# Kernel optimization log

Measured on AMD Instinct MI355X. Metric: run time of the kernel, lower is better.

## Reference

```python
import jax, jax.numpy as jnp
import numpy as np


def _diff_x(x, r):
    left = x[:, r:2 * r + 1]
    middle = x[:, 2 * r + 1:] - x[:, :-2 * r - 1]
    right = x[:, -1:] - x[:, -2 * r - 1:-r - 1]
    return jnp.concatenate([left, middle, right], axis=1)


def _diff_y(x, r):
    left = x[:, :, r:2 * r + 1]
    middle = x[:, :, 2 * r + 1:] - x[:, :, :-2 * r - 1]
    right = x[:, :, -1:] - x[:, :, -2 * r - 1:-r - 1]
    return jnp.concatenate([left, middle, right], axis=2)


def _box_filter(x, r):
    # Sliding box sum via cumsum+diff along H then W (NHWC)
    return _diff_y(jnp.cumsum(_diff_x(jnp.cumsum(x, axis=1), r), axis=2), r)


def setup_inputs() -> dict:
    key = jax.random.key(0)
    k1, k2 = jax.random.split(key)
    B, H, W, C = 4, 1024, 1024, 4
    I = jax.random.uniform(k1, (B, H, W, C), dtype=jnp.float32)
    p = jax.random.uniform(k2, (B, H, W, C), dtype=jnp.float32)
    return {"I": I, "p": p, "r": 40}


def reference(I, p, r):
    eps = 1e-08
    _, H, W, _ = I.shape
    N = _box_filter(jnp.ones((1, H, W, 1), dtype=I.dtype), r)  # box area per pixel
    mean_I = _box_filter(I, r) / N
    mean_p = _box_filter(p, r) / N
    cov_Ip = _box_filter(I * p, r) / N - mean_I * mean_p
    var_I = _box_filter(I * I, r) / N - mean_I * mean_I
    A = cov_Ip / (var_I + eps)
    b = mean_p - A * mean_I
    mean_A = _box_filter(A, r) / N
    mean_b = _box_filter(b, r) / N
    q = mean_A * I + mean_b
    return q
```

## Files before the change

kernel.cpp:

```cpp
#include <hip/hip_runtime.h>
#include <hip/hip_fp16.h>


#define HD 1024
#define WD 1024
#define ROW4 WD
#define IMG4 ((size_t)HD * ROW4)
#define IMGF (IMG4 * 4)
#define BH 16
#define NB (HD / BH)
#define CH 16
#define NCH (HD / CH)
#define TPB 256
#define PPT 4
#define PFXN 1153
#define EPS 1e-8f

__device__ __forceinline__ int idx4(int p) { return p + (p >> 3); }

__device__ __forceinline__ void barrier_lds() {
    asm volatile("s_waitcnt lgkmcnt(0)" ::: "memory");
    __builtin_amdgcn_s_barrier();
}

struct H4 { __half2 lo, hi; };

__device__ __forceinline__ H4 pack4(float4 v) {
    H4 h; h.lo = __floats2half2_rn(v.x, v.y); h.hi = __floats2half2_rn(v.z, v.w);
    return h;
}
__device__ __forceinline__ float4 unpack4(H4 h) {
    float2 l = __half22float2(h.lo), u = __half22float2(h.hi);
    return make_float4(l.x, l.y, u.x, u.y);
}
__device__ __forceinline__ float4 packAB(H4 a, H4 b) {
    union { H4 h[2]; float4 f; } u; u.h[0] = a; u.h[1] = b; return u.f;
}
__device__ __forceinline__ float4 f4add(float4 a, float4 b) {
    return make_float4(a.x + b.x, a.y + b.y, a.z + b.z, a.w + b.w);
}
__device__ __forceinline__ float4 f4sub(float4 a, float4 b) {
    return make_float4(a.x - b.x, a.y - b.y, a.z - b.z, a.w - b.w);
}
__device__ __forceinline__ float4 f4s(float4 a, float s) {
    return make_float4(a.x * s, a.y * s, a.z * s, a.w * s);
}
__device__ __forceinline__ float4 f4mul(float4 a, float4 b) {
    return make_float4(a.x * b.x, a.y * b.y, a.z * b.z, a.w * b.w);
}
__device__ __forceinline__ float4 shup4(float4 v, int d) {
    return make_float4(__shfl_up(v.x, d), __shfl_up(v.y, d), __shfl_up(v.z, d), __shfl_up(v.w, d));
}
__device__ __forceinline__ int band_of(int bx) {
    return (bx >> 3) + (bx & 7) * 8;
}

__global__ __launch_bounds__(TPB, 2) void kchunk(
    const float4* __restrict__ I4, const float4* __restrict__ P4,
    float4* __restrict__ Sc)
{
    const int cb = blockIdx.x;
    const int t = threadIdx.x;
    const size_t imgb = (size_t)blockIdx.y * IMG4;
    const float4* Ib = I4 + imgb + PPT * t;
    const float4* Pb = P4 + imgb + PPT * t;
    const float4 z4 = make_float4(0.f, 0.f, 0.f, 0.f);

    float4 sI[PPT], sp[PPT], sIp[PPT], sII[PPT];
    #pragma unroll
    for (int i = 0; i < PPT; ++i) { sI[i] = z4; sp[i] = z4; sIp[i] = z4; sII[i] = z4; }

    const int j0 = cb * CH;
    for (int j = j0; j < j0 + CH; j += 4) {
        float4 a[4][PPT], c[4][PPT];
        #pragma unroll
        for (int k = 0; k < 4; ++k) {
            const float4* Ir = Ib + (size_t)(j + k) * ROW4;
            const float4* Pr = Pb + (size_t)(j + k) * ROW4;
            #pragma unroll
            for (int i = 0; i < PPT; ++i) { a[k][i] = Ir[i]; c[k][i] = Pr[i]; }
        }
        #pragma unroll
        for (int k = 0; k < 4; ++k)
            #pragma unroll
            for (int i = 0; i < PPT; ++i) {
                sI[i] = f4add(sI[i], a[k][i]);
                sp[i] = f4add(sp[i], c[k][i]);
                sIp[i] = f4add(sIp[i], f4mul(a[k][i], c[k][i]));
                sII[i] = f4add(sII[i], f4mul(a[k][i], a[k][i]));
            }
    }

    const size_t fstride = (size_t)NCH * ROW4;
    float4* S = Sc + (size_t)blockIdx.y * 4 * fstride + (size_t)cb * ROW4 + PPT * t;
    #pragma unroll
    for (int i = 0; i < PPT; ++i) {
        S[i] = sI[i];
        S[fstride + i] = sp[i];
        S[2 * fstride + i] = sIp[i];
        S[3 * fstride + i] = sII[i];
    }
}

__device__ __forceinline__ void scan4d(
    float4 (*pl)[PFXN], float4 (*wt)[4],
    const float4* s0, const float4* s1, const float4* s2, const float4* s3,
    int t, int lane, int wv)
{
    const float4 z4 = make_float4(0.f, 0.f, 0.f, 0.f);
    float4 p0[PPT], p1[PPT], p2[PPT], p3[PPT];
    p0[0] = s0[0]; p1[0] = s1[0]; p2[0] = s2[0]; p3[0] = s3[0];
    #pragma unroll
    for (int i = 1; i < PPT; ++i) {
        p0[i] = f4add(p0[i-1], s0[i]); p1[i] = f4add(p1[i-1], s1[i]);
        p2[i] = f4add(p2[i-1], s2[i]); p3[i] = f4add(p3[i-1], s3[i]);
    }
    float4 i0 = p0[3], i1 = p1[3], i2 = p2[3], i3 = p3[3];
    #pragma unroll
    for (int d = 1; d < 64; d <<= 1) {
        float4 t0 = shup4(i0, d), t1 = shup4(i1, d), t2 = shup4(i2, d), t3 = shup4(i3, d);
        if (lane >= d) {
            i0 = f4add(i0, t0); i1 = f4add(i1, t1);
            i2 = f4add(i2, t2); i3 = f4add(i3, t3);
        }
    }
    float4 e0 = shup4(i0, 1), e1 = shup4(i1, 1), e2 = shup4(i2, 1), e3 = shup4(i3, 1);
    if (lane == 0) { e0 = z4; e1 = z4; e2 = z4; e3 = z4; }
    if (lane == 63) { wt[wv][0] = i0; wt[wv][1] = i1; wt[wv][2] = i2; wt[wv][3] = i3; }
    barrier_lds();
    for (int wq = 0; wq < wv; ++wq) {
        e0 = f4add(e0, wt[wq][0]); e1 = f4add(e1, wt[wq][1]);
        e2 = f4add(e2, wt[wq][2]); e3 = f4add(e3, wt[wq][3]);
    }
    if (t == 0) {
        pl[0][idx4(0)] = z4; pl[1][idx4(0)] = z4;
        pl[2][idx4(0)] = z4; pl[3][idx4(0)] = z4;
    }
    #pragma unroll
    for (int i = 0; i < PPT; ++i) {
        int p = PPT * t + 1 + i;
        pl[0][idx4(p)] = f4add(e0, p0[i]);
        pl[1][idx4(p)] = f4add(e1, p1[i]);
        pl[2][idx4(p)] = f4add(e2, p2[i]);
        pl[3][idx4(p)] = f4add(e3, p3[i]);
    }
    barrier_lds();
}

__device__ __forceinline__ void scan2d(
    float4 (*pl)[PFXN], float4 (*wt)[2],
    const float4* s0, const float4* s1, int t, int lane, int wv)
{
    const float4 z4 = make_float4(0.f, 0.f, 0.f, 0.f);
    float4 p0[PPT], p1[PPT];
    p0[0] = s0[0]; p1[0] = s1[0];
    #pragma unroll
    for (int i = 1; i < PPT; ++i) {
        p0[i] = f4add(p0[i-1], s0[i]); p1[i] = f4add(p1[i-1], s1[i]);
    }
    float4 i0 = p0[3], i1 = p1[3];
    #pragma unroll
    for (int d = 1; d < 64; d <<= 1) {
        float4 t0 = shup4(i0, d), t1 = shup4(i1, d);
        if (lane >= d) { i0 = f4add(i0, t0); i1 = f4add(i1, t1); }
    }
    float4 e0 = shup4(i0, 1), e1 = shup4(i1, 1);
    if (lane == 0) { e0 = z4; e1 = z4; }
    if (lane == 63) { wt[wv][0] = i0; wt[wv][1] = i1; }
    barrier_lds();
    for (int wq = 0; wq < wv; ++wq) {
        e0 = f4add(e0, wt[wq][0]); e1 = f4add(e1, wt[wq][1]);
    }
    if (t == 0) { pl[0][idx4(0)] = z4; pl[1][idx4(0)] = z4; }
    #pragma unroll
    for (int i = 0; i < PPT; ++i) {
        int p = PPT * t + 1 + i;
        pl[0][idx4(p)] = f4add(e0, p0[i]);
        pl[1][idx4(p)] = f4add(e1, p1[i]);
    }
    barrier_lds();
}

__global__ __launch_bounds__(TPB, 1) void kfusedAB(
    const float4* __restrict__ I4, const float4* __restrict__ P4,
    const float4* __restrict__ Sc,
    H4* __restrict__ Aout, H4* __restrict__ Bout,
    const int* __restrict__ rptr)
{
    __shared__ float4 pl[2][4][PFXN];
    __shared__ float4 wt[2][4][4];
    const int r = *rptr;
    const int t = threadIdx.x, lane = t & 63, wv = t >> 6;
    const int h0 = band_of(blockIdx.x) * BH;
    const size_t imgb = (size_t)blockIdx.y * IMG4;
    const float4* Ib = I4 + imgb + PPT * t;
    const float4* Pb = P4 + imgb + PPT * t;
    const size_t fstride = (size_t)NCH * ROW4;
    const float4* Scimg = Sc + (size_t)blockIdx.y * 4 * fstride + PPT * t;
    H4* Ao = Aout + imgb;
    H4* Bo = Bout + imgb;
    const float4 z4 = make_float4(0.f, 0.f, 0.f, 0.f);

    float4 sI[PPT], sp[PPT], sIp[PPT], sII[PPT];
    #pragma unroll
    for (int i = 0; i < PPT; ++i) { sI[i] = z4; sp[i] = z4; sIp[i] = z4; sII[i] = z4; }

    auto rawRows = [&](int a, int b) {
        int j = a;
        for (; j + 3 <= b; j += 4) {
            float4 aa[4][PPT], cc[4][PPT];
            #pragma unroll
            for (int k = 0; k < 4; ++k) {
                const float4* Ir = Ib + (size_t)(j + k) * ROW4;
                const float4* Pr = Pb + (size_t)(j + k) * ROW4;
                #pragma unroll
                for (int i = 0; i < PPT; ++i) { aa[k][i] = Ir[i]; cc[k][i] = Pr[i]; }
            }
            #pragma unroll
            for (int k = 0; k < 4; ++k)
                #pragma unroll
                for (int i = 0; i < PPT; ++i) {
                    sI[i] = f4add(sI[i], aa[k][i]);
                    sp[i] = f4add(sp[i], cc[k][i]);
                    sIp[i] = f4add(sIp[i], f4mul(aa[k][i], cc[k][i]));
                    sII[i] = f4add(sII[i], f4mul(aa[k][i], aa[k][i]));
                }
        }
        for (; j <= b; ++j) {
            const float4* Ir = Ib + (size_t)j * ROW4;
            const float4* Pr = Pb + (size_t)j * ROW4;
            #pragma unroll
            for (int i = 0; i < PPT; ++i) {
                float4 a1 = Ir[i], c1 = Pr[i];
                sI[i] = f4add(sI[i], a1); sp[i] = f4add(sp[i], c1);
                sIp[i] = f4add(sIp[i], f4mul(a1, c1));
                sII[i] = f4add(sII[i], f4mul(a1, a1));
            }
        }
    };

    int lo = h0 - r; if (lo < 0) lo = 0;
    int hi = h0 + r; if (hi > HD - 1) hi = HD - 1;
    int cb0 = (lo + CH - 1) / CH;
    int cb1 = (hi + 1) / CH - 1;
    if (cb0 > cb1) {
        rawRows(lo, hi);
    } else {
        if (lo < cb0 * CH) rawRows(lo, cb0 * CH - 1);
        for (int cb = cb0; cb <= cb1; ++cb) {
            const float4* S = Scimg + (size_t)cb * ROW4;
            float4 v0[PPT], v1[PPT], v2[PPT], v3[PPT];
            #pragma unroll
            for (int i = 0; i < PPT; ++i) {
                v0[i] = S[i];
                v1[i] = S[fstride + i];
                v2[i] = S[2 * fstride + i];
                v3[i] = S[3 * fstride + i];
            }
            #pragma unroll
            for (int i = 0; i < PPT; ++i) {
                sI[i] = f4add(sI[i], v0[i]);
                sp[i] = f4add(sp[i], v1[i]);
                sIp[i] = f4add(sIp[i], v2[i]);
                sII[i] = f4add(sII[i], v3[i]);
            }
        }
        if (hi >= (cb1 + 1) * CH) rawRows((cb1 + 1) * CH, hi);
    }

    for (int h = h0; h < h0 + BH; ++h) {
        const int buf = h & 1;
        int ja = h + 1 + r, js = h - r;
        float wa  = (ja <= HD - 1) ? 1.f : 0.f;
        float wsb = (js >= 0) ? 1.f : 0.f;
        int jac = (ja <= HD - 1) ? ja : HD - 1;
        int jsc = (js >= 0) ? js : 0;
        const float4* Iar = Ib + (size_t)jac * ROW4;
        const float4* Par = Pb + (size_t)jac * ROW4;
        const float4* Isr = Ib + (size_t)jsc * ROW4;
        const float4* Psr = Pb + (size_t)jsc * ROW4;
        float4 La[PPT], Ca[PPT], Ls[PPT], Cs[PPT];
        #pragma unroll
        for (int i = 0; i < PPT; ++i) {
            La[i] = Iar[i]; Ca[i] = Par[i];
            Ls[i] = Isr[i]; Cs[i] = Psr[i];
        }

        int hl = h - r; if (hl < 0) hl = 0;
        int hh = h + r; if (hh > HD - 1) hh = HD - 1;
        const float cntH = (float)(hh - hl + 1);

        scan4d(pl[buf], wt[buf], sI, sp, sIp, sII, t, lane, wv);

        H4 av[PPT], bv[PPT];
        #pragma unroll
        for (int i = 0; i < PPT; ++i) {
            int wp = PPT * t + i;
            int wl = wp - r; if (wl < 0) wl = 0;
            int wh2 = wp + r; if (wh2 > WD - 1) wh2 = WD - 1;
            float invN = 1.f / ((float)(wh2 - wl + 1) * cntH);
            int iA = idx4(wh2 + 1), iB = idx4(wl);
            float4 mI  = f4s(f4sub(pl[buf][0][iA], pl[buf][0][iB]), invN);
            float4 mp  = f4s(f4sub(pl[buf][1][iA], pl[buf][1][iB]), invN);
            float4 mIp = f4s(f4sub(pl[buf][2][iA], pl[buf][2][iB]), invN);
            float4 mII = f4s(f4sub(pl[buf][3][iA], pl[buf][3][iB]), invN);
            float4 cov = f4sub(mIp, f4mul(mI, mp));
            float4 var = f4sub(mII, f4mul(mI, mI));
            float4 Av = make_float4(cov.x / (var.x + EPS), cov.y / (var.y + EPS),
                                    cov.z / (var.z + EPS), cov.w / (var.w + EPS));
            float4 Bv = f4sub(mp, f4mul(Av, mI));
            av[i] = pack4(Av); bv[i] = pack4(Bv);
        }
        {
            float4* Arow = (float4*)(Ao + (size_t)h * ROW4 + PPT * t);
            float4* Brow = (float4*)(Bo + (size_t)h * ROW4 + PPT * t);
            Arow[0] = packAB(av[0], av[1]); Arow[1] = packAB(av[2], av[3]);
            Brow[0] = packAB(bv[0], bv[1]); Brow[1] = packAB(bv[2], bv[3]);
        }

        #pragma unroll
        for (int i = 0; i < PPT; ++i) {
            float4 A1 = f4s(La[i], wa),  C1 = f4s(Ca[i], wa);
            float4 A2 = f4s(Ls[i], wsb), C2 = f4s(Cs[i], wsb);
            sI[i] = f4add(f4sub(sI[i], A2), A1);
            sp[i] = f4add(f4sub(sp[i], C2), C1);
            sIp[i] = f4add(sIp[i], f4sub(f4mul(A1, C1), f4mul(A2, C2)));
            sII[i] = f4add(sII[i], f4sub(f4mul(A1, A1), f4mul(A2, A2)));
        }
    }
}

__global__ __launch_bounds__(TPB, 1) void kfusedQ(
    const H4* __restrict__ Ain, const H4* __restrict__ Bin,
    const float4* __restrict__ I4, float4* __restrict__ Qout,
    const int* __restrict__ rptr)
{
    __shared__ float4 pl[2][2][PFXN];
    __shared__ float4 wt[2][4][2];
    const int r = *rptr;
    const int t = threadIdx.x, lane = t & 63, wv = t >> 6;
    const int h0 = band_of(blockIdx.x) * BH;
    const size_t imgb = (size_t)blockIdx.y * IMG4;
    const H4* Abp = Ain + imgb + PPT * t;
    const H4* Bbp = Bin + imgb + PPT * t;
    const float4* Ib = I4 + imgb + PPT * t;
    float4* Qo = Qout + imgb;
    const float4 z4 = make_float4(0.f, 0.f, 0.f, 0.f);

    float4 sA[PPT], sB[PPT];
    #pragma unroll
    for (int i = 0; i < PPT; ++i) { sA[i] = z4; sB[i] = z4; }

    int lo = h0 - r; if (lo < 0) lo = 0;
    int hi = h0 + r; if (hi > HD - 1) hi = HD - 1;
    int j = lo;
    for (; j + 3 <= hi; j += 4) {
        H4 a[4][PPT], b[4][PPT];
        #pragma unroll
        for (int k = 0; k < 4; ++k) {
            const H4* Ar = Abp + (size_t)(j + k) * ROW4;
            const H4* Br = Bbp + (size_t)(j + k) * ROW4;
            #pragma unroll
            for (int i = 0; i < PPT; ++i) { a[k][i] = Ar[i]; b[k][i] = Br[i]; }
        }
        #pragma unroll
        for (int k = 0; k < 4; ++k)
            #pragma unroll
            for (int i = 0; i < PPT; ++i) {
                sA[i] = f4add(sA[i], unpack4(a[k][i]));
                sB[i] = f4add(sB[i], unpack4(b[k][i]));
            }
    }
    for (; j <= hi; ++j) {
        const H4* Ar = Abp + (size_t)j * ROW4;
        const H4* Br = Bbp + (size_t)j * ROW4;
        #pragma unroll
        for (int i = 0; i < PPT; ++i) {
            sA[i] = f4add(sA[i], unpack4(Ar[i]));
            sB[i] = f4add(sB[i], unpack4(Br[i]));
        }
    }

    for (int h = h0; h < h0 + BH; ++h) {
        const int buf = h & 1;
        int ja = h + 1 + r, js = h - r;
        float wa  = (ja <= HD - 1) ? 1.f : 0.f;
        float wsb = (js >= 0) ? 1.f : 0.f;
        int jac = (ja <= HD - 1) ? ja : HD - 1;
        int jsc = (js >= 0) ? js : 0;
        const H4* Aar = Abp + (size_t)jac * ROW4;
        const H4* Bar = Bbp + (size_t)jac * ROW4;
        const H4* Asr = Abp + (size_t)jsc * ROW4;
        const H4* Bsr = Bbp + (size_t)jsc * ROW4;
        const float4* Irow = Ib + (size_t)h * ROW4;
        H4 La[PPT], Lb[PPT], Sa[PPT], Sb[PPT];
        float4 iv[PPT];
        #pragma unroll
        for (int i = 0; i < PPT; ++i) {
            La[i] = Aar[i]; Lb[i] = Bar[i];
            Sa[i] = Asr[i]; Sb[i] = Bsr[i];
            iv[i] = Irow[i];
        }

        int hl = h - r; if (hl < 0) hl = 0;
        int hh = h + r; if (hh > HD - 1) hh = HD - 1;
        const float cntH = (float)(hh - hl + 1);

        scan2d(pl[buf], wt[buf], sA, sB, t, lane, wv);

        float4* Qrow = Qo + (size_t)h * ROW4 + PPT * t;
        #pragma unroll
        for (int i = 0; i < PPT; ++i) {
            int wp = PPT * t + i;
            int wl = wp - r; if (wl < 0) wl = 0;
            int wh2 = wp + r; if (wh2 > WD - 1) wh2 = WD - 1;
            float invN = 1.f / ((float)(wh2 - wl + 1) * cntH);
            int iA = idx4(wh2 + 1), iB = idx4(wl);
            float4 mA = f4s(f4sub(pl[buf][0][iA], pl[buf][0][iB]), invN);
            float4 mB = f4s(f4sub(pl[buf][1][iA], pl[buf][1][iB]), invN);
            Qrow[i] = make_float4(mA.x * iv[i].x + mB.x, mA.y * iv[i].y + mB.y,
                                  mA.z * iv[i].z + mB.z, mA.w * iv[i].w + mB.w);
        }

        #pragma unroll
        for (int i = 0; i < PPT; ++i) {
            float4 A1 = f4s(unpack4(La[i]), wa);
            float4 B1 = f4s(unpack4(Lb[i]), wa);
            float4 A2 = f4s(unpack4(Sa[i]), wsb);
            float4 B2 = f4s(unpack4(Sb[i]), wsb);
            sA[i] = f4add(f4sub(sA[i], A2), A1);
            sB[i] = f4add(f4sub(sB[i], B2), B1);
        }
    }
}

extern "C" void kernel_launch(void* const* d_in, const int* in_sizes, int n_in,
                              void* d_out, int out_size, void* d_ws, size_t ws_size,
                              hipStream_t stream)
{
    const float* I = (const float*)d_in[0];
    const float* P = (const float*)d_in[1];
    const int* rptr = (const int*)d_in[2];
    float* out = (float*)d_out;

    const int Bn = (int)(in_sizes[0] / IMGF);
    const size_t chunkBytes = (size_t)4 * NCH * ROW4 * sizeof(float4);
    const size_t perBatch = 2 * IMG4 * sizeof(H4) + chunkBytes;

    int nbChunk = (int)(ws_size / perBatch);
    if (nbChunk < 1) nbChunk = 1;
    if (nbChunk > Bn) nbChunk = Bn;

    for (int b0 = 0; b0 < Bn; b0 += nbChunk) {
        const int nb = (b0 + nbChunk <= Bn) ? nbChunk : (Bn - b0);
        H4* Ah = (H4*)d_ws;
        H4* Bh = Ah + (size_t)nb * IMG4;
        float4* Sc = (float4*)(Bh + (size_t)nb * IMG4);
        const float4* Ib = (const float4*)(I + (size_t)b0 * IMGF);
        const float4* Pb = (const float4*)(P + (size_t)b0 * IMGF);
        float4* ob = (float4*)(out + (size_t)b0 * IMGF);

        kchunk<<<dim3(NCH, nb), TPB, 0, stream>>>(Ib, Pb, Sc);
        kfusedAB<<<dim3(NB, nb), TPB, 0, stream>>>(Ib, Pb, Sc, Ah, Bh, rptr);
        kfusedQ<<<dim3(NB, nb), TPB, 0, stream>>>(Ah, Bh, Ib, ob, rptr);
    }
}
```

Baseline: 210.4 us.

## Emit per-band column sums of A and B to shortcut kfusedQ window init

kfusedAB now accumulates fp32 column sums of A and B over its 16-row band and writes them to a new workspace buffer. kfusedQ builds its initial vertical window sum from these per-band partial sums plus raw rows only at the unaligned ends, instead of reading about 2r+1 fp16 rows. This cuts the initial-window read traffic in kfusedQ. It costs extra workspace, an extra write per AB block, and a small numeric difference because the band sums use unrounded fp32 A/B while the sliding updates use fp16 values.

```diff
diff --git a/kernel.cpp b/kernel.cpp
--- a/kernel.cpp
+++ b/kernel.cpp
@@ -185,13 +185,15 @@
     const float4* __restrict__ I4, const float4* __restrict__ P4,
     const float4* __restrict__ Sc,
     H4* __restrict__ Aout, H4* __restrict__ Bout,
+    float4* __restrict__ ScAB,
     const int* __restrict__ rptr)
 {
     __shared__ float4 pl[2][4][PFXN];
     __shared__ float4 wt[2][4][4];
     const int r = *rptr;
     const int t = threadIdx.x, lane = t & 63, wv = t >> 6;
-    const int h0 = band_of(blockIdx.x) * BH;
+    const int band = band_of(blockIdx.x);
+    const int h0 = band * BH;
     const size_t imgb = (size_t)blockIdx.y * IMG4;
     const float4* Ib = I4 + imgb + PPT * t;
     const float4* Pb = P4 + imgb + PPT * t;
@@ -202,8 +204,12 @@
     const float4 z4 = make_float4(0.f, 0.f, 0.f, 0.f);
 
     float4 sI[PPT], sp[PPT], sIp[PPT], sII[PPT];
-    #pragma unroll
-    for (int i = 0; i < PPT; ++i) { sI[i] = z4; sp[i] = z4; sIp[i] = z4; sII[i] = z4; }
+    float4 cA[PPT], cB[PPT];
+    #pragma unroll
+    for (int i = 0; i < PPT; ++i) {
+        sI[i] = z4; sp[i] = z4; sIp[i] = z4; sII[i] = z4;
+        cA[i] = z4; cB[i] = z4;
+    }
 
     auto rawRows = [&](int a, int b) {
         int j = a;
@@ -309,6 +315,8 @@
             float4 Av = make_float4(cov.x / (var.x + EPS), cov.y / (var.y + EPS),
                                     cov.z / (var.z + EPS), cov.w / (var.w + EPS));
             float4 Bv = f4sub(mp, f4mul(Av, mI));
+            cA[i] = f4add(cA[i], Av);
+            cB[i] = f4add(cB[i], Bv);
             av[i] = pack4(Av); bv[i] = pack4(Bv);
         }
         {
@@ -328,10 +336,21 @@
             sII[i] = f4add(sII[i], f4sub(f4mul(A1, A1), f4mul(A2, A2)));
         }
     }
+
+    {
+        const size_t f2 = (size_t)NCH * ROW4;
+        float4* S2 = ScAB + (size_t)blockIdx.y * 2 * f2 + (size_t)band * ROW4 + PPT * t;
+        #pragma unroll
+        for (int i = 0; i < PPT; ++i) {
+            S2[i] = cA[i];
+            S2[f2 + i] = cB[i];
+        }
+    }
 }
 
 __global__ __launch_bounds__(TPB, 1) void kfusedQ(
     const H4* __restrict__ Ain, const H4* __restrict__ Bin,
+    const float4* __restrict__ ScAB,
     const float4* __restrict__ I4, float4* __restrict__ Qout,
     const int* __restrict__ rptr)
 {
@@ -343,6 +362,8 @@
     const size_t imgb = (size_t)blockIdx.y * IMG4;
     const H4* Abp = Ain + imgb + PPT * t;
     const H4* Bbp = Bin + imgb + PPT * t;
+    const size_t f2 = (size_t)NCH * ROW4;
+    const float4* S2img = ScAB + (size_t)blockIdx.y * 2 * f2 + PPT * t;
     const float4* Ib = I4 + imgb + PPT * t;
     float4* Qo = Qout + imgb;
     const float4 z4 = make_float4(0.f, 0.f, 0.f, 0.f);
@@ -351,34 +372,59 @@
     #pragma unroll
     for (int i = 0; i < PPT; ++i) { sA[i] = z4; sB[i] = z4; }
 
+    auto rawRows = [&](int a, int b) {
+        int j = a;
+        for (; j + 3 <= b; j += 4) {
+            H4 aa[4][PPT], bb[4][PPT];
+            #pragma unroll
+            for (int k = 0; k < 4; ++k) {
+                const H4* Ar = Abp + (size_t)(j + k) * ROW4;
+                const H4* Br = Bbp + (size_t)(j + k) * ROW4;
+                #pragma unroll
+                for (int i = 0; i < PPT; ++i) { aa[k][i] = Ar[i]; bb[k][i] = Br[i]; }
+            }
+            #pragma unroll
+            for (int k = 0; k < 4; ++k)
+                #pragma unroll
+                for (int i = 0; i < PPT; ++i) {
+                    sA[i] = f4add(sA[i], unpack4(aa[k][i]));
+                    sB[i] = f4add(sB[i], unpack4(bb[k][i]));
+                }
+        }
+        for (; j <= b; ++j) {
+            const H4* Ar = Abp + (size_t)j * ROW4;
+            const H4* Br = Bbp + (size_t)j * ROW4;
+            #pragma unroll
+            for (int i = 0; i < PPT; ++i) {
+                sA[i] = f4add(sA[i], unpack4(Ar[i]));
+                sB[i] = f4add(sB[i], unpack4(Br[i]));
+            }
+        }
+    };
+
     int lo = h0 - r; if (lo < 0) lo = 0;
     int hi = h0 + r; if (hi > HD - 1) hi = HD - 1;
-    int j = lo;
-    for (; j + 3 <= hi; j += 4) {
-        H4 a[4][PPT], b[4][PPT];
-        #pragma unroll
-        for (int k = 0; k < 4; ++k) {
-            const H4* Ar = Abp + (size_t)(j + k) * ROW4;
-            const H4* Br = Bbp + (size_t)(j + k) * ROW4;
-            #pragma unroll
-            for (int i = 0; i < PPT; ++i) { a[k][i] = Ar[i]; b[k][i] = Br[i]; }
-        }
-        #pragma unroll
-        for (int k = 0; k < 4; ++k)
-            #pragma unroll
-            for (int i = 0; i < PPT; ++i) {
-                sA[i] = f4add(sA[i], unpack4(a[k][i]));
-                sB[i] = f4add(sB[i], unpack4(b[k][i]));
-            }
-    }
-    for (; j <= hi; ++j) {
-        const H4* Ar = Abp + (size_t)j * ROW4;
-        const H4* Br = Bbp + (size_t)j * ROW4;
-        #pragma unroll
-        for (int i = 0; i < PPT; ++i) {
-            sA[i] = f4add(sA[i], unpack4(Ar[i]));
-            sB[i] = f4add(sB[i], unpack4(Br[i]));
-        }
+    int cb0 = (lo + CH - 1) / CH;
+    int cb1 = (hi + 1) / CH - 1;
+    if (cb0 > cb1) {
+        rawRows(lo, hi);
+    } else {
+        if (lo < cb0 * CH) rawRows(lo, cb0 * CH - 1);
+        for (int cb = cb0; cb <= cb1; ++cb) {
+            const float4* S = S2img + (size_t)cb * ROW4;
+            float4 v0[PPT], v1[PPT];
+            #pragma unroll
+            for (int i = 0; i < PPT; ++i) {
+                v0[i] = S[i];
+                v1[i] = S[f2 + i];
+            }
+            #pragma unroll
+            for (int i = 0; i < PPT; ++i) {
+                sA[i] = f4add(sA[i], v0[i]);
+                sB[i] = f4add(sB[i], v1[i]);
+            }
+        }
+        if (hi >= (cb1 + 1) * CH) rawRows((cb1 + 1) * CH, hi);
     }
 
     for (int h = h0; h < h0 + BH; ++h) {
@@ -444,8 +490,9 @@
     float* out = (float*)d_out;
 
     const int Bn = (int)(in_sizes[0] / IMGF);
-    const size_t chunkBytes = (size_t)4 * NCH * ROW4 * sizeof(float4);
-    const size_t perBatch = 2 * IMG4 * sizeof(H4) + chunkBytes;
+    const size_t chunkBytes  = (size_t)4 * NCH * ROW4 * sizeof(float4);
+    const size_t chunkABytes = (size_t)2 * NCH * ROW4 * sizeof(float4);
+    const size_t perBatch = 2 * IMG4 * sizeof(H4) + chunkBytes + chunkABytes;
 
     int nbChunk = (int)(ws_size / perBatch);
     if (nbChunk < 1) nbChunk = 1;
@@ -456,12 +503,13 @@
         H4* Ah = (H4*)d_ws;
         H4* Bh = Ah + (size_t)nb * IMG4;
         float4* Sc = (float4*)(Bh + (size_t)nb * IMG4);
+        float4* ScAB = Sc + (size_t)nb * 4 * NCH * ROW4;
         const float4* Ib = (const float4*)(I + (size_t)b0 * IMGF);
         const float4* Pb = (const float4*)(P + (size_t)b0 * IMGF);
         float4* ob = (float4*)(out + (size_t)b0 * IMGF);
 
         kchunk<<<dim3(NCH, nb), TPB, 0, stream>>>(Ib, Pb, Sc);
-        kfusedAB<<<dim3(NB, nb), TPB, 0, stream>>>(Ib, Pb, Sc, Ah, Bh, rptr);
-        kfusedQ<<<dim3(NB, nb), TPB, 0, stream>>>(Ah, Bh, Ib, ob, rptr);
-    }
-}
+        kfusedAB<<<dim3(NB, nb), TPB, 0, stream>>>(Ib, Pb, Sc, Ah, Bh, ScAB, rptr);
+        kfusedQ<<<dim3(NB, nb), TPB, 0, stream>>>(Ah, Bh, ScAB, Ib, ob, rptr);
+    }
+}
```

New measurement: 180.1 us (median of 2 runs). 14.4% less time.
